# Kernel tuning notes

Hardware: AMD Instinct MI355X
Metric: run time of the kernel (lower is better)

Reference implementation:

```python
import jax, jax.numpy as jnp
import numpy as np

B, S, D_MODEL, HEADS, DK = 2, 2048, 1024, 16, 64


def setup_inputs() -> dict:
    key = jax.random.key(0)
    ks = jax.random.split(key, 7)
    scale = 0.02
    return {
        "query": jax.random.normal(ks[0], (B, S, D_MODEL), jnp.float32),
        "key": jax.random.normal(ks[1], (B, S, D_MODEL), jnp.float32),
        "value": jax.random.normal(ks[2], (B, S, D_MODEL), jnp.float32),
        "Wq": jax.random.normal(ks[3], (D_MODEL, HEADS * DK), jnp.float32) * scale,
        "bq": jax.random.normal(ks[4], (HEADS * DK,), jnp.float32) * scale,
        "Wo": jax.random.normal(ks[5], (HEADS * DK, D_MODEL), jnp.float32) * scale,
        "bo": jax.random.normal(ks[6], (D_MODEL,), jnp.float32) * scale,
    }


def reference(query, key, value, Wq, bq, Wo, bo):
    # NOTE: faithful to the original code, which (buggily) uses _W_q to
    # project query, key AND value, and scales by sqrt(seq_len), not sqrt(d_k).
    seq_len = key.shape[1]

    def split_heads(x):
        # [B,S,H*DK] -> [H,B,S,DK]; torch chunk(dim=-1)+cat(dim=0) stacks head h
        # (slice h*DK:(h+1)*DK) at batch block h.
        p = x @ Wq + bq
        b, s, _ = p.shape
        return p.reshape(b, s, HEADS, DK).transpose(2, 0, 1, 3)

    q = split_heads(query)   # [H,B,S,DK]
    k = split_heads(key)
    v = split_heads(value)

    inv_scale = jnp.float32(1.0 / np.sqrt(seq_len))
    scores = jnp.einsum("hbqd,hbkd->hbqk", q, k) * inv_scale  # [H,B,S,S]
    attn = jax.nn.softmax(scores, axis=-1)
    out = jnp.einsum("hbqk,hbkd->hbqd", attn, v)  # [H,B,S,DK]
    # inverse of chunk(dim=0)+cat(dim=-1): [H,B,S,DK] -> [B,S,H*DK]
    out = out.transpose(1, 2, 0, 3).reshape(query.shape[0], query.shape[1], HEADS * DK)
    return out @ Wo + bo
```

## Files before the change

kernel.cpp:

```cpp
#include <hip/hip_runtime.h>

#define DEVI __device__ __forceinline__

typedef short short4_t __attribute__((ext_vector_type(4)));
typedef short short8_t __attribute__((ext_vector_type(8)));
typedef __bf16 bf16x8 __attribute__((ext_vector_type(8)));
typedef float f32x4 __attribute__((ext_vector_type(4)));

DEVI short f2bf(float f) {
    union { float f; unsigned u; } v; v.f = f;
    unsigned r = (v.u + 0x7fffu + ((v.u >> 16) & 1u)) >> 16;
    return (short)r;
}

DEVI unsigned pack_ru(float a, float b) {
    union { float f; unsigned u; } x, y; x.f = a; y.f = b;
    return __builtin_amdgcn_perm(y.u + 0x8000u, x.u + 0x8000u, 0x07060302u);
}

DEVI void g2lds16(const short* g, short* l) {
    __builtin_amdgcn_global_load_lds(
        (const __attribute__((address_space(1))) void*)g,
        (__attribute__((address_space(3))) void*)l, 16, 0, 0);
}

__global__ __launch_bounds__(256) void prepw_kernel(const float* __restrict__ Wq,
                                                    short* __restrict__ WqT,
                                                    const float* __restrict__ Wo,
                                                    short* __restrict__ WoT) {
    __shared__ short T[64][65];
    const int which = blockIdx.x;
    const int t = threadIdx.x;
    const float* W = (which < 256) ? Wq : Wo;
    short* Wt      = (which < 256) ? WqT : WoT;
    const int bxx = which & 255;
    const int kt = (bxx & 15) * 64, nt = (bxx >> 4) * 64;
#pragma unroll
    for (int r = 0; r < 4; ++r) {
        int kl = (t >> 4) + 16 * r;
        int n0 = (t & 15) * 4;
        f32x4 f = *(const f32x4*)(W + (size_t)(kt + kl) * 1024 + nt + n0);
#pragma unroll
        for (int j = 0; j < 4; ++j) T[n0 + j][kl] = f2bf(f[j]);
    }
    __syncthreads();
#pragma unroll
    for (int r = 0; r < 2; ++r) {
        int nl = (t >> 3) + 32 * r;
        int k0 = (t & 7) * 8;
        short8_t vv;
#pragma unroll
        for (int j = 0; j < 8; ++j) vv[j] = T[nl][k0 + j];
        *(short8_t*)(Wt + (size_t)(nt + nl) * 1024 + kt + k0) = vv;
    }
}

template <typename OutT>
__global__ __launch_bounds__(256) void gemm_qkv_kernel(const float* __restrict__ q,
                                                       const float* __restrict__ kk,
                                                       const float* __restrict__ v,
                                                       const short* __restrict__ Bt,
                                                       const float* __restrict__ bias,
                                                       OutT* __restrict__ C,
                                                       float qscale) {
    constexpr int K = 1024, N = 1024;
    __shared__ __align__(16) short As[2][128 * 32];
    __shared__ __align__(16) short Bs[2][128 * 32];
    const int tid  = threadIdx.x;
    const int lane = tid & 63, wave = tid >> 6;
    const int quad = lane >> 4, l16 = lane & 15;
    const int row0 = blockIdx.x * 128, col0 = blockIdx.y * 128;
    const int wm = (wave >> 1) * 64, wn = (wave & 1) * 64;
    const int srow = lane >> 2;
    const int scol = (lane & 3) * 8;
    const float* Af = (row0 < 4096) ? (q  + (size_t)row0 * K)
                    : (row0 < 8192) ? (kk + (size_t)(row0 - 4096) * K)
                                    : (v  + (size_t)(row0 - 8192) * K);
    const float oscale = (row0 < 4096) ? qscale : 1.0f;
    f32x4 acc[4][4] = {};
    f32x4 ar[2][2];

#define LOADA(k0) do {                                                                  \
        _Pragma("unroll")                                                               \
        for (int r = 0; r < 2; ++r) {                                                   \
            int row = r * 64 + wave * 16 + srow;                                        \
            ar[r][0] = *(const f32x4*)(Af + (size_t)row * K + (k0) + scol);             \
            ar[r][1] = *(const f32x4*)(Af + (size_t)row * K + (k0) + scol + 4);         \
        }                                                                               \
    } while (0)
#define STAGEB(bi, k0) do {                                                             \
        _Pragma("unroll")                                                               \
        for (int r = 0; r < 2; ++r) {                                                   \
            int rb = r * 64 + wave * 16;                                                \
            g2lds16(Bt + (size_t)(col0 + rb + srow) * K + (k0) + scol, &Bs[bi][rb * 32]); \
        }                                                                               \
    } while (0)
#define WRITEA(bi) do {                                                                 \
        _Pragma("unroll")                                                               \
        for (int r = 0; r < 2; ++r) {                                                   \
            int row = r * 64 + wave * 16 + srow;                                        \
            union { unsigned u[4]; short8_t s8; } w;                                    \
            w.u[0] = pack_ru(ar[r][0][0], ar[r][0][1]);                                 \
            w.u[1] = pack_ru(ar[r][0][2], ar[r][0][3]);                                 \
            w.u[2] = pack_ru(ar[r][1][0], ar[r][1][1]);                                 \
            w.u[3] = pack_ru(ar[r][1][2], ar[r][1][3]);                                 \
            *(short8_t*)&As[bi][row * 32 + scol] = w.s8;                                \
        }                                                                               \
    } while (0)

    LOADA(0);
    STAGEB(0, 0);
    WRITEA(0);
    __syncthreads();
    int buf = 0;
    for (int k0 = 0; k0 < K; k0 += 32) {
        const bool more = (k0 + 32 < K);
        if (more) {
            LOADA(k0 + 32);
            STAGEB(buf ^ 1, k0 + 32);
        }
        bf16x8 af[4], bfr[4];
#pragma unroll
        for (int mi = 0; mi < 4; ++mi) af[mi]  = *(const bf16x8*)&As[buf][(wm + mi * 16 + l16) * 32 + quad * 8];
#pragma unroll
        for (int ni = 0; ni < 4; ++ni) bfr[ni] = *(const bf16x8*)&Bs[buf][(wn + ni * 16 + l16) * 32 + quad * 8];
#pragma unroll
        for (int mi = 0; mi < 4; ++mi)
#pragma unroll
            for (int ni = 0; ni < 4; ++ni)
                acc[mi][ni] = __builtin_amdgcn_mfma_f32_16x16x32_bf16(af[mi], bfr[ni], acc[mi][ni], 0, 0, 0);
        if (more) WRITEA(buf ^ 1);
        __syncthreads();
        buf ^= 1;
    }
#undef LOADA
#undef STAGEB
#undef WRITEA
#pragma unroll
    for (int mi = 0; mi < 4; ++mi) {
#pragma unroll
        for (int ni = 0; ni < 4; ++ni) {
            int col = col0 + wn + ni * 16 + l16;
            float bv = bias[col];
#pragma unroll
            for (int i = 0; i < 4; ++i) {
                int row = row0 + wm + mi * 16 + quad * 4 + i;
                float val = (acc[mi][ni][i] + bv) * oscale;
                C[(size_t)row * N + col] = (OutT)f2bf(val);
            }
        }
    }
}

__global__ __launch_bounds__(256) void gemm_bt64_kernel(const short* __restrict__ A,
                                                        const short* __restrict__ Bt,
                                                        const float* __restrict__ bias,
                                                        float* __restrict__ C,
                                                        int M, int N, int K) {
    __shared__ __align__(16) short As[2][64 * 32];
    __shared__ __align__(16) short Bs[2][128 * 32];
    const int tid  = threadIdx.x;
    const int lane = tid & 63, wave = tid >> 6;
    const int quad = lane >> 4, l16 = lane & 15;
    const int row0 = blockIdx.x * 64, col0 = blockIdx.y * 128;
    const int wn = wave * 32;
    const int srow = lane >> 2;
    const int scol = (lane & 3) * 8;
    f32x4 acc[4][2] = {};
    {
        int rb = wave * 16;
        g2lds16(A + (size_t)(row0 + rb + srow) * K + scol, &As[0][rb * 32]);
#pragma unroll
        for (int r = 0; r < 2; ++r) {
            int rb2 = r * 64 + wave * 16;
            g2lds16(Bt + (size_t)(col0 + rb2 + srow) * K + scol, &Bs[0][rb2 * 32]);
        }
    }
    __syncthreads();
    int buf = 0;
    for (int k0 = 0; k0 < K; k0 += 32) {
        if (k0 + 32 < K) {
            int rb = wave * 16;
            g2lds16(A + (size_t)(row0 + rb + srow) * K + k0 + 32 + scol, &As[buf ^ 1][rb * 32]);
#pragma unroll
            for (int r = 0; r < 2; ++r) {
                int rb2 = r * 64 + wave * 16;
                g2lds16(Bt + (size_t)(col0 + rb2 + srow) * K + k0 + 32 + scol, &Bs[buf ^ 1][rb2 * 32]);
            }
        }
        bf16x8 af[4], bfr[2];
#pragma unroll
        for (int mi = 0; mi < 4; ++mi) af[mi]  = *(const bf16x8*)&As[buf][(mi * 16 + l16) * 32 + quad * 8];
#pragma unroll
        for (int ni = 0; ni < 2; ++ni) bfr[ni] = *(const bf16x8*)&Bs[buf][(wn + ni * 16 + l16) * 32 + quad * 8];
#pragma unroll
        for (int mi = 0; mi < 4; ++mi)
#pragma unroll
            for (int ni = 0; ni < 2; ++ni)
                acc[mi][ni] = __builtin_amdgcn_mfma_f32_16x16x32_bf16(af[mi], bfr[ni], acc[mi][ni], 0, 0, 0);
        __syncthreads();
        buf ^= 1;
    }
#pragma unroll
    for (int mi = 0; mi < 4; ++mi) {
#pragma unroll
        for (int ni = 0; ni < 2; ++ni) {
            int col = col0 + wn + ni * 16 + l16;
            float bv = bias[col];
#pragma unroll
            for (int i = 0; i < 4; ++i) {
                int row = row0 + mi * 16 + quad * 4 + i;
                C[(size_t)row * N + col] = acc[mi][ni][i] + bv;
            }
        }
    }
}

__global__ __launch_bounds__(256) void transpose_v_kernel(const short* __restrict__ Pv,
                                                          short* __restrict__ VT) {
    __shared__ short T[64][65];
    const int t = threadIdx.x;
    const int hb = blockIdx.x, st = blockIdx.y * 64;
    const int h = hb >> 1, b = hb & 1;
#pragma unroll
    for (int r = 0; r < 2; ++r) {
        int sl = (t >> 3) + 32 * r;
        short8_t v = *(const short8_t*)(Pv + (size_t)(b * 2048 + st + sl) * 1024 + h * 64 + (t & 7) * 8);
#pragma unroll
        for (int j = 0; j < 8; ++j) T[(t & 7) * 8 + j][sl] = v[j];
    }
    __syncthreads();
#pragma unroll
    for (int r = 0; r < 2; ++r) {
        int dl = (t >> 3) + 32 * r;
        short8_t v;
#pragma unroll
        for (int j = 0; j < 8; ++j) v[j] = T[dl][(t & 7) * 8 + j];
        *(short8_t*)(VT + ((size_t)hb * 64 + dl) * 2048 + st + (t & 7) * 8) = v;
    }
}

__global__ __launch_bounds__(256, 2) void attn_kernel(const short* __restrict__ P,
                                                      const short* __restrict__ VT,
                                                      short* __restrict__ O) {
    constexpr int LDK = 72;
    constexpr int LDV = 136;
    constexpr int LDO = 72;
    union SmemU {
        struct { short Ks[2][128 * LDK]; short Vs[2][64 * LDV]; } s;
        short OT[128 * LDO];
    };
    __shared__ __align__(16) SmemU sm;

    const int t = threadIdx.x;
    const int lane = t & 63, wave = t >> 6;
    const int quad = lane >> 4, l16 = lane & 15;
    const int bx = blockIdx.x;
    const int xcd = bx & 7, bi = bx >> 3;
    const int hb = xcd * 4 + (bi & 3), qt = bi >> 2;
    const int h = hb >> 1, b = hb & 1;
    const short* Pq  = P + (size_t)(b * 2048 + qt * 128) * 1024 + h * 64;
    const short* Pk  = P + (size_t)(4096 + b * 2048) * 1024 + h * 64;
    const short* VTh = VT + (size_t)hb * 64 * 2048;
    const int wq = wave * 32;

    bf16x8 qf[2][2];
#pragma unroll
    for (int miq = 0; miq < 2; ++miq)
#pragma unroll
        for (int kh = 0; kh < 2; ++kh)
            qf[miq][kh] = *(const bf16x8*)(Pq + (size_t)(wq + miq * 16 + l16) * 1024 + kh * 32 + quad * 8);

    bf16x8 ones;
#pragma unroll
    for (int j = 0; j < 8; ++j) ones[j] = (__bf16)1.0f;

    f32x4 oacc[4][2] = {};
    f32x4 osum[2] = {};

    const int krow = t >> 3, kc8 = (t & 7) * 8;
    const int kj = krow & 7, kq = krow >> 3;
    const int lrow32 = (kj >= 4 ? 16 + (kj - 4) : kj) + kq * 4;
    const int vrow = t >> 4, vc8 = (t & 15) * 8;

    short8_t kreg[4], vreg[4];
#pragma unroll
    for (int it = 0; it < 4; ++it) {
        kreg[it] = *(const short8_t*)(Pk + (size_t)(it * 32 + krow) * 1024 + kc8);
        vreg[it] = *(const short8_t*)(VTh + (size_t)(it * 16 + vrow) * 2048 + vc8);
    }

    for (int tile = 0; tile < 16; ++tile) {
        const int buf = tile & 1;
        short* Ksb = sm.s.Ks[buf];
        short* Vsb = sm.s.Vs[buf];
#pragma unroll
        for (int it = 0; it < 4; ++it) {
            *(short8_t*)&Ksb[(it * 32 + lrow32) * LDK + kc8] = kreg[it];
            *(short8_t*)&Vsb[(it * 16 + vrow) * LDV + vc8] = vreg[it];
        }
        __syncthreads();
        if (tile + 1 < 16) {
            int kv0 = (tile + 1) * 128;
#pragma unroll
            for (int it = 0; it < 4; ++it) {
                kreg[it] = *(const short8_t*)(Pk + (size_t)(kv0 + it * 32 + krow) * 1024 + kc8);
                vreg[it] = *(const short8_t*)(VTh + (size_t)(it * 16 + vrow) * 2048 + kv0 + vc8);
            }
        }
#pragma unroll
        for (int p = 0; p < 4; ++p) {
            bf16x8 aA0 = *(const bf16x8*)&Ksb[(p * 32 + l16) * LDK + quad * 8];
            bf16x8 aA1 = *(const bf16x8*)&Ksb[(p * 32 + l16) * LDK + 32 + quad * 8];
            bf16x8 aB0 = *(const bf16x8*)&Ksb[(p * 32 + 16 + l16) * LDK + quad * 8];
            bf16x8 aB1 = *(const bf16x8*)&Ksb[(p * 32 + 16 + l16) * LDK + 32 + quad * 8];
            bf16x8 vA[4];
#pragma unroll
            for (int di = 0; di < 4; ++di)
                vA[di] = *(const bf16x8*)&Vsb[(di * 16 + l16) * LDV + p * 32 + quad * 8];
            __builtin_amdgcn_s_setprio(1);
#pragma unroll
            for (int miq = 0; miq < 2; ++miq) {
                f32x4 sA = {}, sB = {};
                sA = __builtin_amdgcn_mfma_f32_16x16x32_bf16(aA0, qf[miq][0], sA, 0, 0, 0);
                sB = __builtin_amdgcn_mfma_f32_16x16x32_bf16(aB0, qf[miq][0], sB, 0, 0, 0);
                sA = __builtin_amdgcn_mfma_f32_16x16x32_bf16(aA1, qf[miq][1], sA, 0, 0, 0);
                sB = __builtin_amdgcn_mfma_f32_16x16x32_bf16(aB1, qf[miq][1], sB, 0, 0, 0);
                float eA0 = __builtin_amdgcn_exp2f(sA[0]);
                float eA1 = __builtin_amdgcn_exp2f(sA[1]);
                float eA2 = __builtin_amdgcn_exp2f(sA[2]);
                float eA3 = __builtin_amdgcn_exp2f(sA[3]);
                float eB0 = __builtin_amdgcn_exp2f(sB[0]);
                float eB1 = __builtin_amdgcn_exp2f(sB[1]);
                float eB2 = __builtin_amdgcn_exp2f(sB[2]);
                float eB3 = __builtin_amdgcn_exp2f(sB[3]);
                union { unsigned u[4]; bf16x8 b8; } pb;
                pb.u[0] = pack_ru(eA0, eA1);
                pb.u[1] = pack_ru(eA2, eA3);
                pb.u[2] = pack_ru(eB0, eB1);
                pb.u[3] = pack_ru(eB2, eB3);
                osum[miq] = __builtin_amdgcn_mfma_f32_16x16x32_bf16(ones, pb.b8, osum[miq], 0, 0, 0);
#pragma unroll
                for (int di = 0; di < 4; ++di)
                    oacc[di][miq] = __builtin_amdgcn_mfma_f32_16x16x32_bf16(vA[di], pb.b8, oacc[di][miq], 0, 0, 0);
            }
            __builtin_amdgcn_s_setprio(0);
        }
    }

    float rinv[2];
#pragma unroll
    for (int miq = 0; miq < 2; ++miq) rinv[miq] = 1.0f / osum[miq][0];

    __syncthreads();

#pragma unroll
    for (int di = 0; di < 4; ++di) {
#pragma unroll
        for (int miq = 0; miq < 2; ++miq) {
            float v0 = oacc[di][miq][0] * rinv[miq];
            float v1 = oacc[di][miq][1] * rinv[miq];
            float v2 = oacc[di][miq][2] * rinv[miq];
            float v3 = oacc[di][miq][3] * rinv[miq];
            uint2 w;
            w.x = pack_ru(v0, v1);
            w.y = pack_ru(v2, v3);
            int q = wq + miq * 16 + l16;
            *(uint2*)&sm.OT[q * LDO + di * 16 + quad * 4] = w;
        }
    }
    __syncthreads();
    {
        const int orow = t >> 1, ocol = (t & 1) * 32;
        short* dst = O + (size_t)(b * 2048 + qt * 128 + orow) * 1024 + h * 64 + ocol;
#pragma unroll
        for (int c = 0; c < 4; ++c)
            *(short8_t*)(dst + c * 8) = *(const short8_t*)&sm.OT[orow * LDO + ocol + c * 8];
    }
}

extern "C" void kernel_launch(void* const* d_in, const int* in_sizes, int n_in,
                              void* d_out, int out_size, void* d_ws, size_t ws_size,
                              hipStream_t stream) {
    (void)in_sizes; (void)n_in; (void)out_size; (void)ws_size;
    const float* q  = (const float*)d_in[0];
    const float* k  = (const float*)d_in[1];
    const float* v  = (const float*)d_in[2];
    const float* Wq = (const float*)d_in[3];
    const float* bq = (const float*)d_in[4];
    const float* Wo = (const float*)d_in[5];
    const float* bo = (const float*)d_in[6];
    float* out = (float*)d_out;

    short* WqT = (short*)d_ws;
    short* WoT = WqT + (size_t)1024 * 1024;
    short* P   = WoT + (size_t)1024 * 1024;
    short* VT  = P + (size_t)12288 * 1024;
    short* O   = VT + (size_t)32 * 64 * 2048;

    const float qscale = 0.022097086912079608f * 1.4426950408889634f;

    prepw_kernel<<<512, 256, 0, stream>>>(Wq, WqT, Wo, WoT);
    gemm_qkv_kernel<short><<<dim3(96, 8), 256, 0, stream>>>(q, k, v, WqT, bq, P, qscale);
    transpose_v_kernel<<<dim3(32, 32), 256, 0, stream>>>(P + (size_t)8192 * 1024, VT);
    attn_kernel<<<512, 256, 0, stream>>>(P, VT, O);
    gemm_bt64_kernel<<<dim3(64, 8), 256, 0, stream>>>(O, WoT, bo, out, 4096, 1024, 1024);
}
```

Before: 206.0 us.

## Fuse V transpose into QKV GEMM epilogue and deepen A-prefetch pipeline

The separate transpose_v_kernel is removed. Blocks that compute the V projection now transpose their tile through LDS and write VT directly, so the P round-trip for V and one kernel launch are gone. The QKV GEMM main loop is also reworked to prefetch A two steps ahead with ping-pong registers, using explicit s_waitcnt and s_barrier in place of __syncthreads. This adds register pressure and relies on hand-tuned vmcnt counts being correct.

Result: slower. 216.3 us (+5.0%).

```diff
diff --git a/kernel.cpp b/kernel.cpp
--- a/kernel.cpp
+++ b/kernel.cpp
@@ -62,10 +62,14 @@
                                                        const short* __restrict__ Bt,
                                                        const float* __restrict__ bias,
                                                        OutT* __restrict__ C,
+                                                       short* __restrict__ VT,
                                                        float qscale) {
     constexpr int K = 1024, N = 1024;
-    __shared__ __align__(16) short As[2][128 * 32];
-    __shared__ __align__(16) short Bs[2][128 * 32];
+    union GU {
+        struct { short As[2][128 * 32]; short Bs[2][128 * 32]; } g;
+        short T[64][136];
+    };
+    __shared__ __align__(16) GU su;
     const int tid  = threadIdx.x;
     const int lane = tid & 63, wave = tid >> 6;
     const int quad = lane >> 4, l16 = lane & 15;
@@ -76,11 +80,10 @@
     const float* Af = (row0 < 4096) ? (q  + (size_t)row0 * K)
                     : (row0 < 8192) ? (kk + (size_t)(row0 - 4096) * K)
                                     : (v  + (size_t)(row0 - 8192) * K);
-    const float oscale = (row0 < 4096) ? qscale : 1.0f;
     f32x4 acc[4][4] = {};
-    f32x4 ar[2][2];
-
-#define LOADA(k0) do {                                                                  \
+    f32x4 arA[2][2], arB[2][2];
+
+#define LOADA(ar, k0) do {                                                              \
         _Pragma("unroll")                                                               \
         for (int r = 0; r < 2; ++r) {                                                   \
             int row = r * 64 + wave * 16 + srow;                                        \
@@ -92,10 +95,10 @@
         _Pragma("unroll")                                                               \
         for (int r = 0; r < 2; ++r) {                                                   \
             int rb = r * 64 + wave * 16;                                                \
-            g2lds16(Bt + (size_t)(col0 + rb + srow) * K + (k0) + scol, &Bs[bi][rb * 32]); \
+            g2lds16(Bt + (size_t)(col0 + rb + srow) * K + (k0) + scol, &su.g.Bs[bi][rb * 32]); \
         }                                                                               \
     } while (0)
-#define WRITEA(bi) do {                                                                 \
+#define WRITEA(bi, ar) do {                                                             \
         _Pragma("unroll")                                                               \
         for (int r = 0; r < 2; ++r) {                                                   \
             int row = r * 64 + wave * 16 + srow;                                        \
@@ -104,50 +107,102 @@
             w.u[1] = pack_ru(ar[r][0][2], ar[r][0][3]);                                 \
             w.u[2] = pack_ru(ar[r][1][0], ar[r][1][1]);                                 \
             w.u[3] = pack_ru(ar[r][1][2], ar[r][1][3]);                                 \
-            *(short8_t*)&As[bi][row * 32 + scol] = w.s8;                                \
+            *(short8_t*)&su.g.As[bi][row * 32 + scol] = w.s8;                           \
         }                                                                               \
     } while (0)
-
-    LOADA(0);
+#define COMPUTE(bi) do {                                                                \
+        bf16x8 af[4], bfr[4];                                                           \
+        _Pragma("unroll")                                                               \
+        for (int mi = 0; mi < 4; ++mi) af[mi]  = *(const bf16x8*)&su.g.As[bi][(wm + mi * 16 + l16) * 32 + quad * 8]; \
+        _Pragma("unroll")                                                               \
+        for (int ni = 0; ni < 4; ++ni) bfr[ni] = *(const bf16x8*)&su.g.Bs[bi][(wn + ni * 16 + l16) * 32 + quad * 8]; \
+        _Pragma("unroll")                                                               \
+        for (int mi = 0; mi < 4; ++mi)                                                  \
+            _Pragma("unroll")                                                           \
+            for (int ni = 0; ni < 4; ++ni)                                              \
+                acc[mi][ni] = __builtin_amdgcn_mfma_f32_16x16x32_bf16(af[mi], bfr[ni], acc[mi][ni], 0, 0, 0); \
+    } while (0)
+#define HALF(arCUR, arNXT, kc) do {                                                     \
+        STAGEB(buf ^ 1, (kc) + 32);                                                     \
+        __builtin_amdgcn_sched_barrier(0);    \
+        LOADA(arNXT, (kc) + 64);                                                        \
+        COMPUTE(buf);                                                                   \
+        WRITEA(buf ^ 1, arCUR);                     \
+        asm volatile("s_waitcnt vmcnt(4) lgkmcnt(0)" ::: "memory");                     \
+        __builtin_amdgcn_s_barrier();                                                   \
+        buf ^= 1;                                                                       \
+    } while (0)
+
+    int buf = 0;
+    LOADA(arA, 0);
     STAGEB(0, 0);
-    WRITEA(0);
-    __syncthreads();
-    int buf = 0;
-    for (int k0 = 0; k0 < K; k0 += 32) {
-        const bool more = (k0 + 32 < K);
-        if (more) {
-            LOADA(k0 + 32);
-            STAGEB(buf ^ 1, k0 + 32);
-        }
-        bf16x8 af[4], bfr[4];
-#pragma unroll
-        for (int mi = 0; mi < 4; ++mi) af[mi]  = *(const bf16x8*)&As[buf][(wm + mi * 16 + l16) * 32 + quad * 8];
-#pragma unroll
-        for (int ni = 0; ni < 4; ++ni) bfr[ni] = *(const bf16x8*)&Bs[buf][(wn + ni * 16 + l16) * 32 + quad * 8];
-#pragma unroll
-        for (int mi = 0; mi < 4; ++mi)
-#pragma unroll
-            for (int ni = 0; ni < 4; ++ni)
-                acc[mi][ni] = __builtin_amdgcn_mfma_f32_16x16x32_bf16(af[mi], bfr[ni], acc[mi][ni], 0, 0, 0);
-        if (more) WRITEA(buf ^ 1);
-        __syncthreads();
-        buf ^= 1;
-    }
+    WRITEA(0, arA);
+    __builtin_amdgcn_sched_barrier(0);
+    LOADA(arA, 32);
+    asm volatile("s_waitcnt vmcnt(4) lgkmcnt(0)" ::: "memory");
+    __builtin_amdgcn_s_barrier();
+
+    for (int k0 = 0; k0 < 960; k0 += 64) {
+        HALF(arA, arB, k0);
+        HALF(arB, arA, k0 + 32);
+    }
+    STAGEB(buf ^ 1, 992);
+    COMPUTE(buf);
+    WRITEA(buf ^ 1, arA);
+    asm volatile("s_waitcnt vmcnt(0) lgkmcnt(0)" ::: "memory");
+    __builtin_amdgcn_s_barrier();
+    buf ^= 1;
+    COMPUTE(buf);
 #undef LOADA
 #undef STAGEB
 #undef WRITEA
-#pragma unroll
-    for (int mi = 0; mi < 4; ++mi) {
-#pragma unroll
-        for (int ni = 0; ni < 4; ++ni) {
-            int col = col0 + wn + ni * 16 + l16;
-            float bv = bias[col];
-#pragma unroll
-            for (int i = 0; i < 4; ++i) {
-                int row = row0 + wm + mi * 16 + quad * 4 + i;
-                float val = (acc[mi][ni][i] + bv) * oscale;
-                C[(size_t)row * N + col] = (OutT)f2bf(val);
-            }
+#undef COMPUTE
+#undef HALF
+
+    if (row0 < 8192) {
+        const float oscale = (row0 < 4096) ? qscale : 1.0f;
+#pragma unroll
+        for (int mi = 0; mi < 4; ++mi) {
+#pragma unroll
+            for (int ni = 0; ni < 4; ++ni) {
+                int col = col0 + wn + ni * 16 + l16;
+                float bv = bias[col];
+#pragma unroll
+                for (int i = 0; i < 4; ++i) {
+                    int row = row0 + wm + mi * 16 + quad * 4 + i;
+                    float val = (acc[mi][ni][i] + bv) * oscale;
+                    C[(size_t)row * N + col] = (OutT)f2bf(val);
+                }
+            }
+        }
+    } else {
+        const int vb = (row0 - 8192) >> 11;
+        const int s_base = (row0 - 8192) & 2047;
+        __syncthreads();
+#pragma unroll
+        for (int h2 = 0; h2 < 2; ++h2) {
+            if ((wave & 1) == h2) {
+#pragma unroll
+                for (int ni = 0; ni < 4; ++ni) {
+                    int cl = ni * 16 + l16;
+                    float bv = bias[col0 + h2 * 64 + cl];
+#pragma unroll
+                    for (int mi = 0; mi < 4; ++mi)
+#pragma unroll
+                        for (int i = 0; i < 4; ++i)
+                            su.T[cl][wm + mi * 16 + quad * 4 + i] = f2bf(acc[mi][ni][i] + bv);
+                }
+            }
+            __syncthreads();
+            {
+                int dl = tid >> 2, sc = (tid & 3) * 32;
+                int hg = (col0 >> 6) + h2;
+                short* dst = VT + ((size_t)(hg * 2 + vb) * 64 + dl) * 2048 + s_base + sc;
+#pragma unroll
+                for (int c = 0; c < 4; ++c)
+                    *(short8_t*)(dst + c * 8) = *(const short8_t*)&su.T[dl][sc + c * 8];
+            }
+            __syncthreads();
         }
     }
 }
@@ -213,30 +268,6 @@
                 C[(size_t)row * N + col] = acc[mi][ni][i] + bv;
             }
         }
-    }
-}
-
-__global__ __launch_bounds__(256) void transpose_v_kernel(const short* __restrict__ Pv,
-                                                          short* __restrict__ VT) {
-    __shared__ short T[64][65];
-    const int t = threadIdx.x;
-    const int hb = blockIdx.x, st = blockIdx.y * 64;
-    const int h = hb >> 1, b = hb & 1;
-#pragma unroll
-    for (int r = 0; r < 2; ++r) {
-        int sl = (t >> 3) + 32 * r;
-        short8_t v = *(const short8_t*)(Pv + (size_t)(b * 2048 + st + sl) * 1024 + h * 64 + (t & 7) * 8);
-#pragma unroll
-        for (int j = 0; j < 8; ++j) T[(t & 7) * 8 + j][sl] = v[j];
-    }
-    __syncthreads();
-#pragma unroll
-    for (int r = 0; r < 2; ++r) {
-        int dl = (t >> 3) + 32 * r;
-        short8_t v;
-#pragma unroll
-        for (int j = 0; j < 8; ++j) v[j] = T[dl][(t & 7) * 8 + j];
-        *(short8_t*)(VT + ((size_t)hb * 64 + dl) * 2048 + st + (t & 7) * 8) = v;
     }
 }
 
@@ -401,8 +432,7 @@
     const float qscale = 0.022097086912079608f * 1.4426950408889634f;
 
     prepw_kernel<<<512, 256, 0, stream>>>(Wq, WqT, Wo, WoT);
-    gemm_qkv_kernel<short><<<dim3(96, 8), 256, 0, stream>>>(q, k, v, WqT, bq, P, qscale);
-    transpose_v_kernel<<<dim3(32, 32), 256, 0, stream>>>(P + (size_t)8192 * 1024, VT);
+    gemm_qkv_kernel<short><<<dim3(96, 8), 256, 0, stream>>>(q, k, v, WqT, bq, P, VT, qscale);
     attn_kernel<<<512, 256, 0, stream>>>(P, VT, O);
     gemm_bt64_kernel<<<dim3(64, 8), 256, 0, stream>>>(O, WoT, bo, out, 4096, 1024, 1024);
 }
```
